# Kernel tuning notes

Hardware: AMD Instinct MI355X
Metric: run time of the kernel (lower is better)

## Reference

```python
import jax, jax.numpy as jnp
import numpy as np

B, N, D, H = 4, 2048, 256, 8
DH = D // H  # 32
EPS = 1e-5


def layernorm(x, g, b):
    mu = jnp.mean(x, axis=-1, keepdims=True)
    var = jnp.mean(jnp.square(x - mu), axis=-1, keepdims=True)
    return (x - mu) * jax.lax.rsqrt(var + EPS) * g + b


def setup_inputs() -> dict:
    key = jax.random.key(0)
    ks = jax.random.split(key, 16)
    s = 1.0 / np.sqrt(D)
    p = lambda k: jax.random.uniform(k, (D, D), jnp.float32, -s, s)
    return {
        "qdt": jax.random.normal(ks[0], (B, N, D), jnp.float32),
        "boxes": jax.random.normal(ks[1], (B, N, D), jnp.float32),
        "mask": jax.random.randint(ks[2], (N, N), 0, 2, jnp.int32),
        "Wq": p(ks[3]), "bq": jnp.zeros((D,), jnp.float32),
        "Wk": p(ks[4]), "bk": jnp.zeros((D,), jnp.float32),
        "Wv": p(ks[5]), "bv": jnp.zeros((D,), jnp.float32),
        "Wo": p(ks[6]), "bo": jnp.zeros((D,), jnp.float32),
        "W1": p(ks[7]), "b1": jnp.zeros((D,), jnp.float32),
        "W2": p(ks[8]), "b2": jnp.zeros((D,), jnp.float32),
        "g1": jnp.ones((D,), jnp.float32), "be1": jnp.zeros((D,), jnp.float32),
        "g2": jnp.ones((D,), jnp.float32), "be2": jnp.zeros((D,), jnp.float32),
    }


def reference(qdt, boxes, mask, Wq, bq, Wk, bk, Wv, bv, Wo, bo,
              W1, b1, W2, b2, g1, be1, g2, be2):
    # q = k = tgt = boxes + qdt  (dropout in eval mode -> identity)
    x = boxes + qdt  # [B,N,D]
    q = (x @ Wq + bq).reshape(B, N, H, DH)
    k = (x @ Wk + bk).reshape(B, N, H, DH)
    v = (x @ Wv + bv).reshape(B, N, H, DH)
    scores = jnp.einsum('bqhd,bkhd->bhqk', q, k) / np.sqrt(DH)
    # masked_fill(mask==0, -inf) then sigmoid  ==  sigmoid gated to 0 where masked
    attn = jnp.where(mask.astype(bool)[None, None, :, :],
                     jax.nn.sigmoid(scores), 0.0)
    o = jnp.einsum('bhqk,bkhd->bqhd', attn, v).reshape(B, N, D)
    attn_out = o @ Wo + bo
    tgt = layernorm(x + attn_out, g1, be1)
    ff = jax.nn.relu(tgt @ W1 + b1) @ W2 + b2
    tgt = layernorm(tgt + ff, g2, be2)
    return tgt
```

## Files before the change

### kernel.cpp

```cpp
#include <hip/hip_runtime.h>
#include <hip/hip_bf16.h>

typedef unsigned short u16;
typedef unsigned int u32;
typedef __attribute__((ext_vector_type(8))) short bf16x8;
typedef __attribute__((ext_vector_type(4))) float f32x4;

#define BB 4
#define NN 2048
#define DD 256
#define HH 8
#define LAMBDA (-0.2550351f)

__device__ inline u16 bfu(float f) {
  __hip_bfloat16 h = __float2bfloat16(f);
  return *reinterpret_cast<u16*>(&h);
}
__device__ inline bf16x8 asfrag(uint4 v) { return __builtin_bit_cast(bf16x8, v); }

__global__ __launch_bounds__(256) void prep_kernel(
    const float* __restrict__ qdt, const float* __restrict__ boxes,
    const int* __restrict__ mask,
    const float* __restrict__ Wq, const float* __restrict__ Wk, const float* __restrict__ Wv,
    const float* __restrict__ Wo, const float* __restrict__ W1, const float* __restrict__ W2,
    const float* __restrict__ bq, const float* __restrict__ bk, const float* __restrict__ bv,
    float* __restrict__ xp, u16* __restrict__ xb, unsigned char* __restrict__ m8,
    u16* __restrict__ wqkvT, u16* __restrict__ woT, u16* __restrict__ w1T, u16* __restrict__ w2T,
    float* __restrict__ bqkv) {
  const int bid = blockIdx.x, t = threadIdx.x;
  if (bid < 2048) {
    int i = bid * 256 + t;
    int row = i >> 6, q = i & 63;
    float4 a = ((const float4*)qdt)[i];
    float4 b = ((const float4*)boxes)[i];
    float4 v = make_float4(a.x + b.x, a.y + b.y, a.z + b.z, a.w + b.w);
    ((ushort4*)xb)[i] = make_ushort4(bfu(v.x), bfu(v.y), bfu(v.z), bfu(v.w));
    float* xr = xp + (size_t)row * 256;
    xr[((4*q+0) & 15) * 16 + ((4*q+0) >> 4)] = v.x;
    xr[((4*q+1) & 15) * 16 + ((4*q+1) >> 4)] = v.y;
    xr[((4*q+2) & 15) * 16 + ((4*q+2) >> 4)] = v.z;
    xr[((4*q+3) & 15) * 16 + ((4*q+3) >> 4)] = v.w;
  } else if (bid < 6144) {
    int i = (bid - 2048) * 256 + t;
    int4 m = ((const int4*)mask)[i];
    ((uchar4*)m8)[i] = make_uchar4((unsigned char)m.x, (unsigned char)m.y,
                                   (unsigned char)m.z, (unsigned char)m.w);
  } else {
    int i = (bid - 6144) * 256 + t;
    if (i < 196608) {
      int n = i >> 8, k = i & 255;
      const float* src = (n < 256) ? Wq : (n < 512 ? Wk : Wv);
      wqkvT[i] = bfu(src[k * 256 + (n & 255)]);
    } else if (i < 262144) {
      int j = i - 196608; int n = j >> 8, k = j & 255;
      woT[j] = bfu(Wo[k * 256 + n]);
    } else if (i < 327680) {
      int j = i - 262144; int n = j >> 8, k = j & 255;
      w1T[j] = bfu(W1[k * 256 + n]);
    } else if (i < 393216) {
      int j = i - 327680; int n = j >> 8, k = j & 255;
      w2T[j] = bfu(W2[k * 256 + n]);
    } else if (i < 393984) {
      int n = i - 393216;
      bqkv[n] = (n < 256) ? bq[n] : (n < 512 ? bk[n - 256] : bv[n - 512]);
    }
  }
}

__global__ __launch_bounds__(256) void gemm_qkvt_kernel(
    const u16* __restrict__ xb, const u16* __restrict__ wqkvT,
    const float* __restrict__ bqkv,
    u16* __restrict__ qout, u16* __restrict__ kout, u16* __restrict__ vtout) {
  __shared__ u16 At[64][264];
  __shared__ u16 Bs[64][264];
  const int bid = blockIdx.x;
  const bool isqk = bid < 1024;
  const u16* A  = isqk ? xb : (wqkvT + 512 * 256);
  const u16* Bt = isqk ? wqkvT : xb;
  const int m0 = isqk ? (bid >> 3) * 64 : ((bid - 1024) >> 7) * 64;
  const int n0 = isqk ? (bid & 7) * 64 : ((bid - 1024) & 127) * 64;
  const int t = threadIdx.x;
  {
    const int row = t >> 2, cb = (t & 3) * 64;
    const u16* ga = A  + (size_t)(m0 + row) * 256 + cb;
    const u16* gb = Bt + (size_t)(n0 + row) * 256 + cb;
#pragma unroll
    for (int i = 0; i < 8; ++i) {
      *(int4*)&At[row][cb + i * 8] = *(const int4*)(ga + i * 8);
      *(int4*)&Bs[row][cb + i * 8] = *(const int4*)(gb + i * 8);
    }
  }
  __syncthreads();
  const int w = t >> 6, l = t & 63, g = l >> 4, c = l & 15;
  f32x4 acc[4] = {};
#pragma unroll
  for (int kk = 0; kk < 256; kk += 32) {
    bf16x8 af = *(const bf16x8*)&At[w * 16 + c][kk + g * 8];
#pragma unroll
    for (int j = 0; j < 4; ++j) {
      bf16x8 bfr = *(const bf16x8*)&Bs[j * 16 + c][kk + g * 8];
      acc[j] = __builtin_amdgcn_mfma_f32_16x16x32_bf16(af, bfr, acc[j], 0, 0, 0);
    }
  }
  if (isqk) {
    if (n0 < 256) {
#pragma unroll
      for (int j = 0; j < 4; ++j)
#pragma unroll
        for (int r = 0; r < 4; ++r) {
          int m = m0 + w * 16 + g * 4 + r, n = n0 + j * 16 + c;
          qout[(size_t)m * 256 + n] = bfu((acc[j][r] + bqkv[n]) * LAMBDA);
        }
    } else {
#pragma unroll
      for (int j = 0; j < 4; ++j)
#pragma unroll
        for (int r = 0; r < 4; ++r) {
          int m = m0 + w * 16 + g * 4 + r, n = n0 + j * 16 + c;
          int ch = n - 256;
          kout[(size_t)((m >> 11) * 8 + (ch >> 5)) * 65536 + (size_t)(m & 2047) * 32 + (ch & 31)]
              = bfu(acc[j][r] + bqkv[n]);
        }
    }
  } else {
#pragma unroll
    for (int j = 0; j < 4; ++j)
#pragma unroll
      for (int r = 0; r < 4; ++r) {
        int m = m0 + w * 16 + g * 4 + r;
        int n = n0 + j * 16 + c;
        vtout[(size_t)m * 8192 + n] = bfu(acc[j][r] + bqkv[512 + m]);
      }
  }
}

__global__ __launch_bounds__(256) void attn_kernel(
    const u16* __restrict__ qb,
    const u16* __restrict__ kb,
    const u16* __restrict__ vtb,
    const unsigned char* __restrict__ m8,
    u16* __restrict__ ob) {
  __shared__ u32 Klds[2][64][20];
  __shared__ u32 Vlds[2][32][36];
  __shared__ u32 Plds[4][16][36];

  const int bid = blockIdx.x;
  const int qt = bid & 31, h = (bid >> 5) & 7, b = bid >> 8;
  const int q0 = qt * 64;
  const int t = threadIdx.x, w = t >> 6, l = t & 63, g = l >> 4, c = l & 15;

  const bf16x8 qf = asfrag(*(const uint4*)(qb + (size_t)(b * NN + q0 + 16 * w + c) * 256 + h * 32 + 8 * g));
  f32x4 oacc[2] = {};

  const int srowK = t >> 2, ssegK = t & 3;
  const int srowV = t >> 3, ssegV = t & 7;
  const u16* kg = kb + (size_t)(b * 8 + h) * 65536 + srowK * 32 + ssegK * 8;
  const u16* vg = vtb + (size_t)(h * 32 + srowV) * 8192 + (size_t)b * NN + ssegV * 8;
  const unsigned char* mrow = m8 + (size_t)(q0 + 16 * w + c) * 2048 + 4 * g;

  uint4 krg = *(const uint4*)kg;
  uint4 vrg = *(const uint4*)vg;
  *(uint4*)&Klds[0][srowK][ssegK * 4] = krg;
  *(uint4*)&Vlds[0][srowV][ssegV * 4] = vrg;
  __syncthreads();

  const f32x4 zf = {0.f, 0.f, 0.f, 0.f};
  u32* Pw = &Plds[w][0][0];

  for (int it = 0; it < 32; ++it) {
    const int cur = it & 1;
    const int kt = it * 64;
    if (it < 31) {
      krg = *(const uint4*)(kg + (size_t)(kt + 64) * 32);
      vrg = *(const uint4*)(vg + kt + 64);
    }
#pragma unroll
    for (int tt = 0; tt < 4; ++tt) {
      bf16x8 kf = asfrag(*(const uint4*)&Klds[cur][16 * tt + c][4 * g]);
      f32x4 s = __builtin_amdgcn_mfma_f32_16x16x32_bf16(kf, qf, zf, 0, 0, 0);
      u32 mdw = *(const u32*)(mrow + kt + 16 * tt);
      float mf0 = (float)(mdw & 0xffu);
      float mf1 = (float)((mdw >> 8) & 0xffu);
      float mf2 = (float)((mdw >> 16) & 0xffu);
      float mf3 = (float)(mdw >> 24);
      float p0 = mf0 * __builtin_amdgcn_rcpf(1.f + __builtin_amdgcn_exp2f(s[0]));
      float p1 = mf1 * __builtin_amdgcn_rcpf(1.f + __builtin_amdgcn_exp2f(s[1]));
      float p2 = mf2 * __builtin_amdgcn_rcpf(1.f + __builtin_amdgcn_exp2f(s[2]));
      float p3 = mf3 * __builtin_amdgcn_rcpf(1.f + __builtin_amdgcn_exp2f(s[3]));
      u32 w0, w1;
      asm("v_cvt_pk_bf16_f32 %0, %1, %2" : "=v"(w0) : "v"(p0), "v"(p1));
      asm("v_cvt_pk_bf16_f32 %0, %1, %2" : "=v"(w1) : "v"(p2), "v"(p3));
      *(uint2*)&Pw[c * 36 + 8 * tt + 2 * g] = make_uint2(w0, w1);
    }
    asm volatile("s_waitcnt lgkmcnt(0)" ::: "memory");
    __builtin_amdgcn_sched_barrier(0);
#pragma unroll
    for (int kk = 0; kk < 2; ++kk) {
      bf16x8 pf = asfrag(*(const uint4*)&Pw[c * 36 + 16 * kk + 4 * g]);
#pragma unroll
      for (int d0 = 0; d0 < 2; ++d0) {
        bf16x8 vf = asfrag(*(const uint4*)&Vlds[cur][16 * d0 + c][16 * kk + 4 * g]);
        oacc[d0] = __builtin_amdgcn_mfma_f32_16x16x32_bf16(pf, vf, oacc[d0], 0, 0, 0);
      }
    }
    if (it < 31) {
      *(uint4*)&Klds[cur ^ 1][srowK][ssegK * 4] = krg;
      *(uint4*)&Vlds[cur ^ 1][srowV][ssegV * 4] = vrg;
    }
    __syncthreads();
  }

  const size_t obase = (size_t)(b * NN + q0 + 16 * w) * 256 + h * 32;
#pragma unroll
  for (int d0 = 0; d0 < 2; ++d0)
#pragma unroll
    for (int r = 0; r < 4; ++r)
      ob[obase + (size_t)(4 * g + r) * 256 + 16 * d0 + c] = bfu(oacc[d0][r]);
}

__global__ __launch_bounds__(256) void tail_kernel(
    const u16* __restrict__ obuf, const u16* __restrict__ woT,
    const u16* __restrict__ w1T, const u16* __restrict__ w2T,
    const float* __restrict__ xp,
    const float* __restrict__ bo, const float* __restrict__ b1, const float* __restrict__ b2,
    const float* __restrict__ g1, const float* __restrict__ be1,
    const float* __restrict__ g2, const float* __restrict__ be2,
    float* __restrict__ out) {
  __shared__ u16 A[32][264];
  __shared__ float PS1[32][4], PS2[32][4];
  const int t = threadIdx.x, w = t >> 6, l = t & 63, g = l >> 4, c = l & 15;
  const int m0 = blockIdx.x * 32;
  const int n0 = w * 64;
  const f32x4 zf4 = {0.f, 0.f, 0.f, 0.f};

  {
    const int srow = t >> 3, sseg = t & 7;
#pragma unroll
    for (int i = 0; i < 4; ++i) {
      uint4 v = *(const uint4*)(obuf + (size_t)(m0 + srow) * 256 + (sseg + 8 * i) * 8);
      *(uint4*)&A[srow][(sseg + 8 * i) * 8] = v;
    }
  }
  __syncthreads();

  f32x4 acc[2][4], t1[2][4];
  float mean[2][4], inv[2][4];

#pragma unroll
  for (int rg = 0; rg < 2; ++rg)
#pragma unroll
    for (int j = 0; j < 4; ++j) acc[rg][j] = zf4;
#pragma unroll
  for (int kk = 0; kk < 256; kk += 32) {
    bf16x8 af0 = *(const bf16x8*)&A[c][kk + 8 * g];
    bf16x8 af1 = *(const bf16x8*)&A[16 + c][kk + 8 * g];
#pragma unroll
    for (int j = 0; j < 4; ++j) {
      bf16x8 bfr = asfrag(*(const uint4*)(woT + (size_t)(n0 + 16 * j + c) * 256 + kk + 8 * g));
      acc[0][j] = __builtin_amdgcn_mfma_f32_16x16x32_bf16(af0, bfr, acc[0][j], 0, 0, 0);
      acc[1][j] = __builtin_amdgcn_mfma_f32_16x16x32_bf16(af1, bfr, acc[1][j], 0, 0, 0);
    }
  }
  {
    float bov[4];
#pragma unroll
    for (int j = 0; j < 4; ++j) bov[j] = bo[n0 + 16 * j + c];
#pragma unroll
    for (int rg = 0; rg < 2; ++rg)
#pragma unroll
      for (int r = 0; r < 4; ++r) {
        const int rl = 16 * rg + 4 * g + r;
        float4 xq = ((const float4*)(xp + (size_t)(m0 + rl) * 256 + c * 16))[w];
        float xa[4] = {xq.x, xq.y, xq.z, xq.w};
        float a1 = 0.f, a2 = 0.f;
#pragma unroll
        for (int j = 0; j < 4; ++j) {
          float z = acc[rg][j][r] + bov[j] + xa[j];
          t1[rg][j][r] = z;
          a1 += z; a2 += z * z;
        }
#pragma unroll
        for (int off = 1; off < 16; off <<= 1) {
          a1 += __shfl_xor(a1, off);
          a2 += __shfl_xor(a2, off);
        }
        if (c == 0) { PS1[rl][w] = a1; PS2[rl][w] = a2; }
      }
  }
  __syncthreads();
#pragma unroll
  for (int rg = 0; rg < 2; ++rg)
#pragma unroll
    for (int r = 0; r < 4; ++r) {
      const int rl = 16 * rg + 4 * g + r;
      float s1 = PS1[rl][0] + PS1[rl][1] + PS1[rl][2] + PS1[rl][3];
      float s2 = PS2[rl][0] + PS2[rl][1] + PS2[rl][2] + PS2[rl][3];
      mean[rg][r] = s1 * (1.f / 256.f);
      inv[rg][r] = rsqrtf(s2 * (1.f / 256.f) - mean[rg][r] * mean[rg][r] + 1e-5f);
    }
#pragma unroll
  for (int j = 0; j < 4; ++j) {
    const int n = n0 + 16 * j + c;
    const float gv = g1[n], bev = be1[n];
#pragma unroll
    for (int rg = 0; rg < 2; ++rg)
#pragma unroll
      for (int r = 0; r < 4; ++r) {
        float v = (t1[rg][j][r] - mean[rg][r]) * inv[rg][r] * gv + bev;
        t1[rg][j][r] = v;
        A[16 * rg + 4 * g + r][n] = bfu(v);
      }
  }
  __syncthreads();

#pragma unroll
  for (int rg = 0; rg < 2; ++rg)
#pragma unroll
    for (int j = 0; j < 4; ++j) acc[rg][j] = zf4;
#pragma unroll
  for (int kk = 0; kk < 256; kk += 32) {
    bf16x8 af0 = *(const bf16x8*)&A[c][kk + 8 * g];
    bf16x8 af1 = *(const bf16x8*)&A[16 + c][kk + 8 * g];
#pragma unroll
    for (int j = 0; j < 4; ++j) {
      bf16x8 bfr = asfrag(*(const uint4*)(w1T + (size_t)(n0 + 16 * j + c) * 256 + kk + 8 * g));
      acc[0][j] = __builtin_amdgcn_mfma_f32_16x16x32_bf16(af0, bfr, acc[0][j], 0, 0, 0);
      acc[1][j] = __builtin_amdgcn_mfma_f32_16x16x32_bf16(af1, bfr, acc[1][j], 0, 0, 0);
    }
  }
  __syncthreads();
#pragma unroll
  for (int j = 0; j < 4; ++j) {
    const int n = n0 + 16 * j + c;
    const float bv = b1[n];
#pragma unroll
    for (int rg = 0; rg < 2; ++rg)
#pragma unroll
      for (int r = 0; r < 4; ++r) {
        float v = acc[rg][j][r] + bv;
        A[16 * rg + 4 * g + r][n] = bfu(v > 0.f ? v : 0.f);
      }
  }
  __syncthreads();

#pragma unroll
  for (int rg = 0; rg < 2; ++rg)
#pragma unroll
    for (int j = 0; j < 4; ++j) acc[rg][j] = zf4;
#pragma unroll
  for (int kk = 0; kk < 256; kk += 32) {
    bf16x8 af0 = *(const bf16x8*)&A[c][kk + 8 * g];
    bf16x8 af1 = *(const bf16x8*)&A[16 + c][kk + 8 * g];
#pragma unroll
    for (int j = 0; j < 4; ++j) {
      bf16x8 bfr = asfrag(*(const uint4*)(w2T + (size_t)(n0 + 16 * j + c) * 256 + kk + 8 * g));
      acc[0][j] = __builtin_amdgcn_mfma_f32_16x16x32_bf16(af0, bfr, acc[0][j], 0, 0, 0);
      acc[1][j] = __builtin_amdgcn_mfma_f32_16x16x32_bf16(af1, bfr, acc[1][j], 0, 0, 0);
    }
  }
  {
    float b2v[4];
#pragma unroll
    for (int j = 0; j < 4; ++j) b2v[j] = b2[n0 + 16 * j + c];
#pragma unroll
    for (int rg = 0; rg < 2; ++rg)
#pragma unroll
      for (int r = 0; r < 4; ++r) {
        const int rl = 16 * rg + 4 * g + r;
        float a1 = 0.f, a2 = 0.f;
#pragma unroll
        for (int j = 0; j < 4; ++j) {
          float z = acc[rg][j][r] + b2v[j] + t1[rg][j][r];
          t1[rg][j][r] = z;
          a1 += z; a2 += z * z;
        }
#pragma unroll
        for (int off = 1; off < 16; off <<= 1) {
          a1 += __shfl_xor(a1, off);
          a2 += __shfl_xor(a2, off);
        }
        if (c == 0) { PS1[rl][w] = a1; PS2[rl][w] = a2; }
      }
  }
  __syncthreads();
#pragma unroll
  for (int rg = 0; rg < 2; ++rg)
#pragma unroll
    for (int r = 0; r < 4; ++r) {
      const int rl = 16 * rg + 4 * g + r;
      float s1 = PS1[rl][0] + PS1[rl][1] + PS1[rl][2] + PS1[rl][3];
      float s2 = PS2[rl][0] + PS2[rl][1] + PS2[rl][2] + PS2[rl][3];
      mean[rg][r] = s1 * (1.f / 256.f);
      inv[rg][r] = rsqrtf(s2 * (1.f / 256.f) - mean[rg][r] * mean[rg][r] + 1e-5f);
    }
#pragma unroll
  for (int j = 0; j < 4; ++j) {
    const int n = n0 + 16 * j + c;
    const float gv = g2[n], bev = be2[n];
#pragma unroll
    for (int rg = 0; rg < 2; ++rg)
#pragma unroll
      for (int r = 0; r < 4; ++r)
        out[(size_t)(m0 + 16 * rg + 4 * g + r) * 256 + n]
            = (t1[rg][j][r] - mean[rg][r]) * inv[rg][r] * gv + bev;
  }
}

extern "C" void kernel_launch(void* const* d_in, const int* in_sizes, int n_in,
                              void* d_out, int out_size, void* d_ws, size_t ws_size,
                              hipStream_t stream) {
  const float* qdt   = (const float*)d_in[0];
  const float* boxes = (const float*)d_in[1];
  const int*   mask  = (const int*)d_in[2];
  const float* Wq = (const float*)d_in[3];
  const float* bq = (const float*)d_in[4];
  const float* Wk = (const float*)d_in[5];
  const float* bk = (const float*)d_in[6];
  const float* Wv = (const float*)d_in[7];
  const float* bv = (const float*)d_in[8];
  const float* Wo = (const float*)d_in[9];
  const float* bo = (const float*)d_in[10];
  const float* W1 = (const float*)d_in[11];
  const float* b1 = (const float*)d_in[12];
  const float* W2 = (const float*)d_in[13];
  const float* b2 = (const float*)d_in[14];
  const float* g1  = (const float*)d_in[15];
  const float* be1 = (const float*)d_in[16];
  const float* g2  = (const float*)d_in[17];
  const float* be2 = (const float*)d_in[18];

  char* ws = (char*)d_ws;
  float* xp    = (float*)(ws + 0);
  u16*   xb    = (u16*)  (ws + 8388608);
  u16*   qbuf  = (u16*)  (ws + 12582912);
  u16*   kbuf  = (u16*)  (ws + 16777216);
  u16*   vtbuf = (u16*)  (ws + 20971520);
  u16*   obuf  = (u16*)  (ws + 25165824);
  u16*   wqkvT = (u16*)  (ws + 46137344);
  u16*   woT   = (u16*)  (ws + 46530560);
  u16*   w1T   = (u16*)  (ws + 46661632);
  u16*   w2T   = (u16*)  (ws + 46792704);
  float* bqkv  = (float*)(ws + 46923776);
  unsigned char* m8 = (unsigned char*)(ws + 46926848);

  prep_kernel<<<7683, 256, 0, stream>>>(qdt, boxes, mask, Wq, Wk, Wv, Wo, W1, W2,
                                        bq, bk, bv, xp, xb, m8,
                                        wqkvT, woT, w1T, w2T, bqkv);
  gemm_qkvt_kernel<<<1536, 256, 0, stream>>>(xb, wqkvT, bqkv, qbuf, kbuf, vtbuf);
  attn_kernel<<<1024, 256, 0, stream>>>(qbuf, kbuf, vtbuf, m8, obuf);
  tail_kernel<<<256, 256, 0, stream>>>(obuf, woT, w1T, w2T, xp,
                                       bo, b1, b2, g1, be1, g2, be2, (float*)d_out);
}
```

Before: 130.2 us.

## Double attention query tile per block and stage mask tiles through swizzled LDS

Each attention block now handles 128 query rows instead of 64, with each wave computing two 16-row query fragments. The K/V tiles loaded into LDS are therefore reused across twice as many queries, halving K/V global traffic. The mask is now loaded cooperatively into double-buffered LDS with a rotated layout to avoid bank conflicts, replacing the old per-thread scattered global reads. The costs are half as many blocks (512), more registers and more LDS per block, which may reduce occupancy and wave-level parallelism.

```diff
diff --git a/kernel.cpp b/kernel.cpp
--- a/kernel.cpp
+++ b/kernel.cpp
@@ -142,26 +142,39 @@
     u16* __restrict__ ob) {
   __shared__ u32 Klds[2][64][20];
   __shared__ u32 Vlds[2][32][36];
-  __shared__ u32 Plds[4][16][36];
+  __shared__ unsigned char Mlds[2][128][64];
+  __shared__ u32 Plds[4][32][36];
 
   const int bid = blockIdx.x;
-  const int qt = bid & 31, h = (bid >> 5) & 7, b = bid >> 8;
-  const int q0 = qt * 64;
+  const int qt = bid & 15, h = (bid >> 4) & 7, b = bid >> 7;
+  const int q0 = qt * 128;
   const int t = threadIdx.x, w = t >> 6, l = t & 63, g = l >> 4, c = l & 15;
 
-  const bf16x8 qf = asfrag(*(const uint4*)(qb + (size_t)(b * NN + q0 + 16 * w + c) * 256 + h * 32 + 8 * g));
-  f32x4 oacc[2] = {};
+  const bf16x8 qf0 = asfrag(*(const uint4*)(qb + (size_t)(b * NN + q0 + 32 * w + c) * 256 + h * 32 + 8 * g));
+  const bf16x8 qf1 = asfrag(*(const uint4*)(qb + (size_t)(b * NN + q0 + 32 * w + 16 + c) * 256 + h * 32 + 8 * g));
+  f32x4 oacc[2][2] = {};
 
   const int srowK = t >> 2, ssegK = t & 3;
   const int srowV = t >> 3, ssegV = t & 7;
+  const int msrow = t >> 1, mhalf = t & 1;
   const u16* kg = kb + (size_t)(b * 8 + h) * 65536 + srowK * 32 + ssegK * 8;
   const u16* vg = vtb + (size_t)(h * 32 + srowV) * 8192 + (size_t)b * NN + ssegV * 8;
-  const unsigned char* mrow = m8 + (size_t)(q0 + 16 * w + c) * 2048 + 4 * g;
+  const unsigned char* mg = m8 + (size_t)(q0 + msrow) * NN + mhalf * 32;
+
+  const int rotM = 8 * (msrow & 7);
+  const int mbA0 = (32 * mhalf + rotM) & 63, mbA1 = (mbA0 + 8) & 63;
+  const int mbB0 = (mbA0 + 16) & 63,         mbB1 = (mbA0 + 24) & 63;
 
   uint4 krg = *(const uint4*)kg;
   uint4 vrg = *(const uint4*)vg;
+  uint4 mrgA = *(const uint4*)mg;
+  uint4 mrgB = *(const uint4*)(mg + 16);
   *(uint4*)&Klds[0][srowK][ssegK * 4] = krg;
   *(uint4*)&Vlds[0][srowV][ssegV * 4] = vrg;
+  *(uint2*)&Mlds[0][msrow][mbA0] = make_uint2(mrgA.x, mrgA.y);
+  *(uint2*)&Mlds[0][msrow][mbA1] = make_uint2(mrgA.z, mrgA.w);
+  *(uint2*)&Mlds[0][msrow][mbB0] = make_uint2(mrgB.x, mrgB.y);
+  *(uint2*)&Mlds[0][msrow][mbB1] = make_uint2(mrgB.z, mrgB.w);
   __syncthreads();
 
   const f32x4 zf = {0.f, 0.f, 0.f, 0.f};
@@ -169,53 +182,75 @@
 
   for (int it = 0; it < 32; ++it) {
     const int cur = it & 1;
-    const int kt = it * 64;
     if (it < 31) {
-      krg = *(const uint4*)(kg + (size_t)(kt + 64) * 32);
-      vrg = *(const uint4*)(vg + kt + 64);
+      const int kt = (it + 1) * 64;
+      krg = *(const uint4*)(kg + (size_t)kt * 32);
+      vrg = *(const uint4*)(vg + kt);
+      mrgA = *(const uint4*)(mg + kt);
+      mrgB = *(const uint4*)(mg + kt + 16);
     }
 #pragma unroll
     for (int tt = 0; tt < 4; ++tt) {
       bf16x8 kf = asfrag(*(const uint4*)&Klds[cur][16 * tt + c][4 * g]);
-      f32x4 s = __builtin_amdgcn_mfma_f32_16x16x32_bf16(kf, qf, zf, 0, 0, 0);
-      u32 mdw = *(const u32*)(mrow + kt + 16 * tt);
-      float mf0 = (float)(mdw & 0xffu);
-      float mf1 = (float)((mdw >> 8) & 0xffu);
-      float mf2 = (float)((mdw >> 16) & 0xffu);
-      float mf3 = (float)(mdw >> 24);
-      float p0 = mf0 * __builtin_amdgcn_rcpf(1.f + __builtin_amdgcn_exp2f(s[0]));
-      float p1 = mf1 * __builtin_amdgcn_rcpf(1.f + __builtin_amdgcn_exp2f(s[1]));
-      float p2 = mf2 * __builtin_amdgcn_rcpf(1.f + __builtin_amdgcn_exp2f(s[2]));
-      float p3 = mf3 * __builtin_amdgcn_rcpf(1.f + __builtin_amdgcn_exp2f(s[3]));
-      u32 w0, w1;
-      asm("v_cvt_pk_bf16_f32 %0, %1, %2" : "=v"(w0) : "v"(p0), "v"(p1));
-      asm("v_cvt_pk_bf16_f32 %0, %1, %2" : "=v"(w1) : "v"(p2), "v"(p3));
-      *(uint2*)&Pw[c * 36 + 8 * tt + 2 * g] = make_uint2(w0, w1);
+      f32x4 s0 = __builtin_amdgcn_mfma_f32_16x16x32_bf16(kf, qf0, zf, 0, 0, 0);
+      f32x4 s1 = __builtin_amdgcn_mfma_f32_16x16x32_bf16(kf, qf1, zf, 0, 0, 0);
+      const int mpos = (16 * tt + 4 * g + 8 * (c & 7)) & 63;
+      u32 mdw0 = *(const u32*)&Mlds[cur][32 * w + c][mpos];
+      u32 mdw1 = *(const u32*)&Mlds[cur][32 * w + 16 + c][mpos];
+      {
+        float p0 = (float)(mdw0 & 0xffu) * __builtin_amdgcn_rcpf(1.f + __builtin_amdgcn_exp2f(s0[0]));
+        float p1 = (float)((mdw0 >> 8) & 0xffu) * __builtin_amdgcn_rcpf(1.f + __builtin_amdgcn_exp2f(s0[1]));
+        float p2 = (float)((mdw0 >> 16) & 0xffu) * __builtin_amdgcn_rcpf(1.f + __builtin_amdgcn_exp2f(s0[2]));
+        float p3 = (float)(mdw0 >> 24) * __builtin_amdgcn_rcpf(1.f + __builtin_amdgcn_exp2f(s0[3]));
+        u32 w0, w1;
+        asm("v_cvt_pk_bf16_f32 %0, %1, %2" : "=v"(w0) : "v"(p0), "v"(p1));
+        asm("v_cvt_pk_bf16_f32 %0, %1, %2" : "=v"(w1) : "v"(p2), "v"(p3));
+        *(uint2*)&Pw[c * 36 + 8 * tt + 2 * g] = make_uint2(w0, w1);
+      }
+      {
+        float p0 = (float)(mdw1 & 0xffu) * __builtin_amdgcn_rcpf(1.f + __builtin_amdgcn_exp2f(s1[0]));
+        float p1 = (float)((mdw1 >> 8) & 0xffu) * __builtin_amdgcn_rcpf(1.f + __builtin_amdgcn_exp2f(s1[1]));
+        float p2 = (float)((mdw1 >> 16) & 0xffu) * __builtin_amdgcn_rcpf(1.f + __builtin_amdgcn_exp2f(s1[2]));
+        float p3 = (float)(mdw1 >> 24) * __builtin_amdgcn_rcpf(1.f + __builtin_amdgcn_exp2f(s1[3]));
+        u32 w0, w1;
+        asm("v_cvt_pk_bf16_f32 %0, %1, %2" : "=v"(w0) : "v"(p0), "v"(p1));
+        asm("v_cvt_pk_bf16_f32 %0, %1, %2" : "=v"(w1) : "v"(p2), "v"(p3));
+        *(uint2*)&Pw[(16 + c) * 36 + 8 * tt + 2 * g] = make_uint2(w0, w1);
+      }
     }
     asm volatile("s_waitcnt lgkmcnt(0)" ::: "memory");
     __builtin_amdgcn_sched_barrier(0);
 #pragma unroll
     for (int kk = 0; kk < 2; ++kk) {
-      bf16x8 pf = asfrag(*(const uint4*)&Pw[c * 36 + 16 * kk + 4 * g]);
+      bf16x8 pf0 = asfrag(*(const uint4*)&Pw[c * 36 + 16 * kk + 4 * g]);
+      bf16x8 pf1 = asfrag(*(const uint4*)&Pw[(16 + c) * 36 + 16 * kk + 4 * g]);
 #pragma unroll
       for (int d0 = 0; d0 < 2; ++d0) {
         bf16x8 vf = asfrag(*(const uint4*)&Vlds[cur][16 * d0 + c][16 * kk + 4 * g]);
-        oacc[d0] = __builtin_amdgcn_mfma_f32_16x16x32_bf16(pf, vf, oacc[d0], 0, 0, 0);
+        oacc[0][d0] = __builtin_amdgcn_mfma_f32_16x16x32_bf16(pf0, vf, oacc[0][d0], 0, 0, 0);
+        oacc[1][d0] = __builtin_amdgcn_mfma_f32_16x16x32_bf16(pf1, vf, oacc[1][d0], 0, 0, 0);
       }
     }
     if (it < 31) {
       *(uint4*)&Klds[cur ^ 1][srowK][ssegK * 4] = krg;
       *(uint4*)&Vlds[cur ^ 1][srowV][ssegV * 4] = vrg;
+      *(uint2*)&Mlds[cur ^ 1][msrow][mbA0] = make_uint2(mrgA.x, mrgA.y);
+      *(uint2*)&Mlds[cur ^ 1][msrow][mbA1] = make_uint2(mrgA.z, mrgA.w);
+      *(uint2*)&Mlds[cur ^ 1][msrow][mbB0] = make_uint2(mrgB.x, mrgB.y);
+      *(uint2*)&Mlds[cur ^ 1][msrow][mbB1] = make_uint2(mrgB.z, mrgB.w);
     }
     __syncthreads();
   }
 
-  const size_t obase = (size_t)(b * NN + q0 + 16 * w) * 256 + h * 32;
-#pragma unroll
-  for (int d0 = 0; d0 < 2; ++d0)
-#pragma unroll
-    for (int r = 0; r < 4; ++r)
-      ob[obase + (size_t)(4 * g + r) * 256 + 16 * d0 + c] = bfu(oacc[d0][r]);
+#pragma unroll
+  for (int f = 0; f < 2; ++f) {
+    const size_t obase = (size_t)(b * NN + q0 + 32 * w + 16 * f) * 256 + h * 32;
+#pragma unroll
+    for (int d0 = 0; d0 < 2; ++d0)
+#pragma unroll
+      for (int r = 0; r < 4; ++r)
+        ob[obase + (size_t)(4 * g + r) * 256 + 16 * d0 + c] = bfu(oacc[f][d0][r]);
+  }
 }
 
 __global__ __launch_bounds__(256) void tail_kernel(
@@ -447,7 +482,7 @@
                                         bq, bk, bv, xp, xb, m8,
                                         wqkvT, woT, w1T, w2T, bqkv);
   gemm_qkvt_kernel<<<1536, 256, 0, stream>>>(xb, wqkvT, bqkv, qbuf, kbuf, vtbuf);
-  attn_kernel<<<1024, 256, 0, stream>>>(qbuf, kbuf, vtbuf, m8, obuf);
+  attn_kernel<<<512, 256, 0, stream>>>(qbuf, kbuf, vtbuf, m8, obuf);
   tail_kernel<<<256, 256, 0, stream>>>(obuf, woT, w1T, w2T, xp,
                                        bo, b1, b2, g1, be1, g2, be2, (float*)d_out);
 }
```

After: 115.5 us. 11.3% less time.
